# Kernel tuning notes

Hardware: AMD Instinct MI355X
Metric: run time of the kernel (lower is better)

## Reference

```python
import jax, jax.numpy as jnp
from jax import lax
import numpy as np

B, C_IN, HW = 4096, 3, 32
D = 256          # feature/output dim
E = 16           # num experts
H = 1024         # expert hidden dim
K = 2            # top-k
NC = 1000        # num classes


def _conv(x, w, b):
    # x: NCHW, w: OIHW, stride 1, SAME padding
    y = lax.conv_general_dilated(x, w, (1, 1), 'SAME',
                                 dimension_numbers=('NCHW', 'OIHW', 'NCHW'))
    return y + b[None, :, None, None]


def _maxpool2(x):
    return lax.reduce_window(x, -jnp.inf, lax.max, (1, 1, 2, 2), (1, 1, 2, 2), 'VALID')


def setup_inputs() -> dict:
    key = jax.random.key(0)
    ks = jax.random.split(key, 16)
    s = lambda *sh: 1.0 / np.sqrt(sh[-2] if len(sh) > 1 else sh[0])
    inp = {
        'x':       jax.random.normal(ks[0], (B, C_IN, HW, HW), jnp.float32),
        'conv1_w': jax.random.normal(ks[1], (32, 3, 3, 3), jnp.float32) * 0.1,
        'conv1_b': jnp.zeros((32,), jnp.float32),
        'conv2_w': jax.random.normal(ks[2], (64, 32, 3, 3), jnp.float32) * 0.05,
        'conv2_b': jnp.zeros((64,), jnp.float32),
        'conv3_w': jax.random.normal(ks[3], (128, 64, 3, 3), jnp.float32) * 0.04,
        'conv3_b': jnp.zeros((128,), jnp.float32),
        'fc_w':    jax.random.normal(ks[4], (128 * 4 * 4, D), jnp.float32) * (1.0 / np.sqrt(2048)),
        'fc_b':    jnp.zeros((D,), jnp.float32),
        'gate_w':  jax.random.normal(ks[5], (D, E), jnp.float32) * (1.0 / np.sqrt(D)),
        'gate_b':  jnp.zeros((E,), jnp.float32),
        'e_w1':    jax.random.normal(ks[6], (E, D, H), jnp.float32) * (1.0 / np.sqrt(D)),
        'e_b1':    jnp.zeros((E, H), jnp.float32),
        'e_w2':    jax.random.normal(ks[7], (E, H, D), jnp.float32) * (1.0 / np.sqrt(H)),
        'e_b2':    jnp.zeros((E, D), jnp.float32),
        'ln_g':    jnp.ones((D,), jnp.float32),
        'ln_b':    jnp.zeros((D,), jnp.float32),
        'out_w':   jax.random.normal(ks[8], (D, NC), jnp.float32) * (1.0 / np.sqrt(D)),
        'out_b':   jnp.zeros((NC,), jnp.float32),
    }
    return inp


def reference(x, conv1_w, conv1_b, conv2_w, conv2_b, conv3_w, conv3_b,
              fc_w, fc_b, gate_w, gate_b, e_w1, e_b1, e_w2, e_b2,
              ln_g, ln_b, out_w, out_b):
    # --- CNN feature extractor: conv -> maxpool -> relu, x3 ---
    h = jax.nn.relu(_maxpool2(_conv(x, conv1_w, conv1_b)))   # [B,32,16,16]
    h = jax.nn.relu(_maxpool2(_conv(h, conv2_w, conv2_b)))   # [B,64,8,8]
    h = jax.nn.relu(_maxpool2(_conv(h, conv3_w, conv3_b)))   # [B,128,4,4]
    feat = h.reshape(h.shape[0], -1) @ fc_w + fc_b           # [B,D]

    # --- Gating: top-k softmax scattered into sparse [B,E] ---
    logits = feat @ gate_w + gate_b                          # [B,E]
    topk_vals, topk_idx = lax.top_k(logits, K)               # [B,K]
    gate_w_k = jax.nn.softmax(topk_vals, axis=-1)            # [B,K]
    gates = jnp.zeros_like(logits).at[jnp.arange(feat.shape[0])[:, None], topk_idx].set(gate_w_k)

    # --- Dense all-expert compute, masked combine (faithful to source) ---
    h1 = jax.nn.relu(jnp.einsum('bd,edh->beh', feat, e_w1) + e_b1[None])   # [B,E,H]
    eo = jnp.einsum('beh,ehd->bed', h1, e_w2) + e_b2[None]                 # [B,E,D]
    moe = jnp.einsum('be,bed->bd', gates, eo)                              # [B,D]

    D_i = gates.mean(axis=0)
    lb_loss = jnp.sum(D_i * jnp.log(D_i + 1e-8))

    # --- LayerNorm(residual) ---
    y = moe + feat
    mu = y.mean(-1, keepdims=True)
    var = y.var(-1, keepdims=True)
    y = (y - mu) / jnp.sqrt(var + 1e-5) * ln_g + ln_b

    out = y @ out_w + out_b                                   # [B,NC]
    return out, lb_loss
```

## Files before the change

kernel.cpp:

```cpp
#include <hip/hip_runtime.h>
#include <hip/hip_bf16.h>

typedef short bf16x8 __attribute__((ext_vector_type(8)));
typedef float f32x4 __attribute__((ext_vector_type(4)));

#define NB   4096
#define NEXP 16
#define DDIM 256
#define HDIM 1024
#define NCLS 1000

#define OFF_B    ((size_t)0)
#define OFF_P0   ((size_t)0)
#define OFF_P1   ((size_t)4194304)
#define OFF_W1TH ((size_t)8388608)
#define OFF_W1TL ((size_t)16777216)
#define OFF_W2TH ((size_t)25165824)
#define OFF_W2TL ((size_t)33554432)
#define OFF_WFCH ((size_t)41943040)
#define OFF_WFCL ((size_t)42991616)
#define OFF_P2   ((size_t)44040192)
#define OFF_P3   ((size_t)48234496)
#define OFF_OWH  ((size_t)52428800)
#define OFF_OWL  ((size_t)53477376)
#define OFF_CHH  ((size_t)67108864)
#define OFF_CHL  ((size_t)83886080)
#define OFF_WBL  ((size_t)67145728)
#define OFF_WA1H ((size_t)67182592)
#define OFF_WA1L ((size_t)67184640)
#define OFF_FEAT ((size_t)100663296)
#define OFF_WAL  ((size_t)100810752)
#define OFF_MOE  ((size_t)104857600)
#define OFF_CNT  ((size_t)109051904)
#define OFF_GSUM ((size_t)109051968)
#define OFF_LROW ((size_t)109052032)
#define OFF_LG   ((size_t)109314176)

__device__ inline unsigned short f2bf(float v) {
  __hip_bfloat16 h = __float2bfloat16(v);
  return *(unsigned short*)&h;
}
__device__ inline float bf2f(unsigned short u) {
  union { unsigned int i; float f; } c; c.i = ((unsigned int)u) << 16; return c.f;
}

__global__ __launch_bounds__(256) void k_wt1b(const float* __restrict__ w,
    unsigned short* __restrict__ oh, unsigned short* __restrict__ ol) {
  int i = blockIdx.x*256 + threadIdx.x;
  if (i >= 1024) return;
  int k = i & 31, oc = i >> 5;
  float v = (k < 27) ? w[oc*27 + k] : 0.f;
  unsigned short h = f2bf(v);
  oh[i] = h;
  ol[i] = f2bf(v - bf2f(h));
}

__global__ __launch_bounds__(256) void k_wt2b(const float* __restrict__ w,
    unsigned short* __restrict__ wBh, unsigned short* __restrict__ wBl) {
  int i = blockIdx.x*256 + threadIdx.x;
  if (i >= 9*64*32) return;
  int ic = i & 31, rem = i >> 5;
  int oc = rem & 63, tap = rem >> 6;
  float v = w[(oc*32 + ic)*9 + tap];
  unsigned short h = f2bf(v);
  wBh[i] = h;
  wBl[i] = f2bf(v - bf2f(h));
}

__global__ __launch_bounds__(256) void k_pack(const float* __restrict__ in,
    unsigned short* __restrict__ oh, unsigned short* __restrict__ ol, int R, int C) {
  __shared__ float tile[64][65];
  const int t = threadIdx.x;
  const int e = blockIdx.z;
  const size_t eb = (size_t)e * R * C;
  const int c0 = blockIdx.x*64, r0 = blockIdx.y*64;
  const int cc = t & 63, r4 = t >> 6;
  #pragma unroll
  for (int j = 0; j < 16; ++j) {
    int rr = r4 + j*4;
    tile[rr][cc] = in[eb + (size_t)(r0+rr)*C + c0 + cc];
  }
  __syncthreads();
  const int K32 = R >> 5;
  #pragma unroll
  for (int j = 0; j < 16; ++j) {
    int idx = t + j*256;
    int jin = idx & 7, lane = (idx >> 3) & 63, ksl = (idx >> 9) & 1, ntl = idx >> 10;
    int kl = ksl*32 + ((lane >> 4) << 3) + jin;
    int nl = ntl*16 + (lane & 15);
    float v = tile[kl][nl];
    unsigned short h = f2bf(v);
    size_t o = eb + ((size_t)(((c0 >> 4) + ntl)*K32 + (r0 >> 5) + ksl)*64 + lane)*8 + jin;
    oh[o] = h;
    ol[o] = f2bf(v - bf2f(h));
  }
}

__global__ __launch_bounds__(256) void k_packo(const float* __restrict__ ow,
    unsigned short* __restrict__ oh, unsigned short* __restrict__ ol) {
  int i = blockIdx.x*256 + threadIdx.x;
  int j = i & 7, lane = (i >> 3) & 63, ks = (i >> 9) & 7, nt = i >> 12;
  int k = ks*32 + ((lane >> 4) << 3) + j;
  int n = nt*16 + (lane & 15);
  float v = (n < NCLS) ? ow[(size_t)k*NCLS + n] : 0.f;
  unsigned short h = f2bf(v);
  oh[i] = h;
  ol[i] = f2bf(v - bf2f(h));
}

__global__ __launch_bounds__(512, 4) void k_conv12(const float* __restrict__ x,
    const unsigned short* __restrict__ wA1h, const unsigned short* __restrict__ wA1l,
    const float* __restrict__ b1,
    const unsigned short* __restrict__ wBh, const unsigned short* __restrict__ wBl,
    const float* __restrict__ b2, float* __restrict__ outB) {
  __shared__ unsigned int xsu[3*34*36];
  __shared__ unsigned short ishB[2][10368];
  __shared__ float bs1[32];
  __shared__ float bs2[64];
  const int t = threadIdx.x;
  const int img = blockIdx.x;
  for (int i = t; i < 3*34*36; i += 512) xsu[i] = 0u;
  {
    unsigned int* z = (unsigned int*)&ishB[0][0];
    for (int i = t; i < 10368; i += 512) z[i] = 0u;
  }
  __syncthreads();
  for (int i = t; i < 3072; i += 512) {
    int ic = i >> 10, rem = i & 1023, y = rem >> 5, xx = rem & 31;
    float v = x[(size_t)img*3072 + i];
    unsigned short h = f2bf(v);
    unsigned short l = f2bf(v - bf2f(h));
    xsu[ic*34*36 + (y+1)*36 + (xx+1)] = ((unsigned int)l << 16) | (unsigned int)h;
  }
  if (t < 32) bs1[t] = b1[t];
  else if (t >= 64 && t < 128) bs2[t-64] = b2[t-64];

  const int lane = t & 63, wvv = t >> 6;
  const int lr = lane & 15, lq = lane >> 4;

  const int oct1 = wvv & 1;
  const bf16x8 a1h = *(const bf16x8*)&wA1h[((oct1*16 + lr) << 5) + lq*8];
  const bf16x8 a1l = *(const bf16x8*)&wA1l[((oct1*16 + lr) << 5) + lq*8];

  int koff[8];
  #pragma unroll
  for (int j = 0; j < 8; ++j) {
    int k = lq*8 + j;
    if (k < 27) {
      int ic = k/9, tap = k - ic*9, dy = tap/3, dx = tap - dy*3;
      koff[j] = ic*34*36 + dy*36 + dx;
    } else koff[j] = -1;
  }
  __syncthreads();

  {
    const int rp  = wvv >> 1;
    const int ly0 = (rp >> 1) << 1;
    const int xh  = rp & 1;
    const int X   = xh*16 + lr;
    for (int ps = 0; ps < 8; ++ps) {
      const int baseA = (ps*4 + ly0)*36 + X;
      union { unsigned int u[4]; bf16x8 v; } bhA, blA, bhB, blB;
      #pragma unroll
      for (int jj = 0; jj < 4; ++jj) {
        unsigned int e0A = (koff[2*jj]   >= 0) ? xsu[koff[2*jj]   + baseA] : 0u;
        unsigned int e1A = (koff[2*jj+1] >= 0) ? xsu[koff[2*jj+1] + baseA] : 0u;
        unsigned int e0B = (koff[2*jj]   >= 0) ? xsu[koff[2*jj]   + baseA + 36] : 0u;
        unsigned int e1B = (koff[2*jj+1] >= 0) ? xsu[koff[2*jj+1] + baseA + 36] : 0u;
        bhA.u[jj] = __builtin_amdgcn_perm(e1A, e0A, 0x05040100u);
        blA.u[jj] = __builtin_amdgcn_perm(e1A, e0A, 0x07060302u);
        bhB.u[jj] = __builtin_amdgcn_perm(e1B, e0B, 0x05040100u);
        blB.u[jj] = __builtin_amdgcn_perm(e1B, e0B, 0x07060302u);
      }
      f32x4 aA = (f32x4){0.f,0.f,0.f,0.f}, aB = (f32x4){0.f,0.f,0.f,0.f};
      aA = __builtin_amdgcn_mfma_f32_16x16x32_bf16(a1h, bhA.v, aA, 0, 0, 0);
      aB = __builtin_amdgcn_mfma_f32_16x16x32_bf16(a1h, bhB.v, aB, 0, 0, 0);
      aA = __builtin_amdgcn_mfma_f32_16x16x32_bf16(a1h, blA.v, aA, 0, 0, 0);
      aB = __builtin_amdgcn_mfma_f32_16x16x32_bf16(a1h, blB.v, aB, 0, 0, 0);
      aA = __builtin_amdgcn_mfma_f32_16x16x32_bf16(a1l, bhA.v, aA, 0, 0, 0);
      aB = __builtin_amdgcn_mfma_f32_16x16x32_bf16(a1l, bhB.v, aB, 0, 0, 0);
      #pragma unroll
      for (int r = 0; r < 4; ++r) {
        float v = fmaxf(aA[r], aB[r]);
        v = fmaxf(v, __shfl_xor(v, 1, 64));
        if ((lr & 1) == 0) {
          int oc = oct1*16 + lq*4 + r;
          int Xp = xh*8 + (lr >> 1);
          int Yp = ps*2 + (ly0 >> 1);
          float m = fmaxf(v + bs1[oc], 0.f);
          unsigned short h = f2bf(m);
          unsigned short l = f2bf(m - bf2f(h));
          int pl = (Yp+1)*18 + (Xp+1);
          int sl = pl*4 + ((oc >> 3) ^ ((pl >> 1) & 3));
          int us = (sl << 3) | (oc & 7);
          ishB[0][us] = h; ishB[1][us] = l;
        }
      }
    }
  }
  __syncthreads();
  {
    const int mtp = (wvv & 1)*2;
    const int rq = wvv >> 1;
    f32x4 acc[2][4];
    #pragma unroll
    for (int i = 0; i < 2; ++i)
      #pragma unroll
      for (int j = 0; j < 4; ++j) acc[i][j] = (f32x4){0.f,0.f,0.f,0.f};
    bf16x8 nAh[2], nAl[2];
    #pragma unroll
    for (int m = 0; m < 2; ++m) {
      int off = (((mtp+m)*16 + lr) << 5) + lq*8;
      nAh[m] = *(const bf16x8*)&wBh[off];
      nAl[m] = *(const bf16x8*)&wBl[off];
    }
    #pragma unroll
    for (int tap = 0; tap < 9; ++tap) {
      bf16x8 ah0 = nAh[0], al0 = nAl[0], ah1 = nAh[1], al1 = nAl[1];
      if (tap < 8) {
        #pragma unroll
        for (int m = 0; m < 2; ++m) {
          int off = (((tap+1)*64 + (mtp+m)*16 + lr) << 5) + lq*8;
          nAh[m] = *(const bf16x8*)&wBh[off];
          nAl[m] = *(const bf16x8*)&wBl[off];
        }
      }
      const int dy = tap/3, dx = tap - dy*3;
      #pragma unroll
      for (int j = 0; j < 4; ++j) {
        int pl = (rq*4 + j + dy)*18 + lr + dx;
        int sl = pl*4 + (lq ^ ((pl >> 1) & 3));
        bf16x8 bh = *(const bf16x8*)&ishB[0][sl << 3];
        bf16x8 bl = *(const bf16x8*)&ishB[1][sl << 3];
        acc[0][j] = __builtin_amdgcn_mfma_f32_16x16x32_bf16(ah0, bh, acc[0][j], 0, 0, 0);
        acc[1][j] = __builtin_amdgcn_mfma_f32_16x16x32_bf16(ah1, bh, acc[1][j], 0, 0, 0);
        acc[0][j] = __builtin_amdgcn_mfma_f32_16x16x32_bf16(ah0, bl, acc[0][j], 0, 0, 0);
        acc[1][j] = __builtin_amdgcn_mfma_f32_16x16x32_bf16(ah1, bl, acc[1][j], 0, 0, 0);
        acc[0][j] = __builtin_amdgcn_mfma_f32_16x16x32_bf16(al0, bh, acc[0][j], 0, 0, 0);
        acc[1][j] = __builtin_amdgcn_mfma_f32_16x16x32_bf16(al1, bh, acc[1][j], 0, 0, 0);
      }
    }
    __syncthreads();
    float* ps2 = (float*)&ishB[0][0];
    #pragma unroll
    for (int m = 0; m < 2; ++m)
      #pragma unroll
      for (int k = 0; k < 2; ++k)
        #pragma unroll
        for (int r = 0; r < 4; ++r) {
          float v = fmaxf(acc[m][2*k][r], acc[m][2*k+1][r]);
          v = fmaxf(v, __shfl_xor(v, 1, 64));
          if ((lr & 1) == 0) {
            int oc = (mtp + m)*16 + lq*4 + r;
            int Y = rq*2 + k, X = lr >> 1;
            ps2[oc*65 + Y*8 + X] = fmaxf(v + bs2[oc], 0.f);
          }
        }
    __syncthreads();
    float* op = outB + (size_t)img*4096;
    #pragma unroll
    for (int jj = 0; jj < 8; ++jj) {
      int i = jj*512 + t;
      op[i] = ps2[(i >> 6)*65 + (i & 63)];
    }
  }
}

__global__ __launch_bounds__(256) void k_wt3b(const float* __restrict__ w,
    unsigned short* __restrict__ wAh, unsigned short* __restrict__ wAl) {
  int i = blockIdx.x*256 + threadIdx.x;
  if (i >= 9*128*64) return;
  int ic = i & 63, rem = i >> 6;
  int oc = rem & 127, tap = rem >> 7;
  float v = w[(oc*64 + ic)*9 + tap];
  unsigned short h = f2bf(v);
  wAh[i] = h;
  wAl[i] = f2bf(v - bf2f(h));
}

__global__ __launch_bounds__(256) void k_conv3(const float* __restrict__ inB,
    const unsigned short* __restrict__ wAh, const unsigned short* __restrict__ wAl,
    const float* __restrict__ bias,
    unsigned short* __restrict__ Chh, unsigned short* __restrict__ Chl) {
  __shared__ unsigned short ish[2][6400];
  const int t = threadIdx.x;
  const int img = blockIdx.x;
  {
    unsigned int* z = (unsigned int*)&ish[0][0];
    #pragma unroll
    for (int j = 0; j < 25; ++j) z[t + 256*j] = 0u;
  }
  __syncthreads();
  {
    const float* src = inB + (size_t)img*4096;
    #pragma unroll
    for (int j = 0; j < 16; ++j) {
      int f = t + 256*j;
      int ic = f >> 6, p = f & 63;
      int pl = ((p >> 3) + 1)*10 + (p & 7) + 1;
      float v = src[f];
      unsigned short h = f2bf(v);
      unsigned short l = f2bf(v - bf2f(h));
      int u = pl*64 + ic;
      int us = (((u >> 3) ^ (pl & 7)) << 3) | (u & 7);
      ish[0][us] = h; ish[1][us] = l;
    }
  }
  __syncthreads();

  const int lane = t & 63, wid = t >> 6;
  const int lr = lane & 15, lq = lane >> 4;
  const int mt0 = wid*2;
  const int yb = lr >> 3, xb = lr & 7;

  f32x4 acc[2][4];
  #pragma unroll
  for (int i = 0; i < 2; ++i)
    #pragma unroll
    for (int j = 0; j < 4; ++j) acc[i][j] = (f32x4){0.f,0.f,0.f,0.f};

  for (int tap = 0; tap < 9; ++tap) {
    const int dy = tap/3, dx = tap - dy*3;
    #pragma unroll
    for (int kc = 0; kc < 2; ++kc) {
      const int kb = kc*32 + lq*8;
      const int wbase = ((tap << 7) << 6) + kb;
      bf16x8 a0h = *(const bf16x8*)&wAh[wbase + ((mt0*16 + lr) << 6)];
      bf16x8 a0l = *(const bf16x8*)&wAl[wbase + ((mt0*16 + lr) << 6)];
      bf16x8 a1h = *(const bf16x8*)&wAh[wbase + (((mt0+1)*16 + lr) << 6)];
      bf16x8 a1l = *(const bf16x8*)&wAl[wbase + (((mt0+1)*16 + lr) << 6)];
      #pragma unroll
      for (int nt = 0; nt < 4; ++nt) {
        const int pl = (2*nt + yb + dy)*10 + xb + dx;
        const int u = pl*64 + kb;
        const int us = (((u >> 3) ^ (pl & 7)) << 3);
        bf16x8 bh = *(const bf16x8*)&ish[0][us];
        bf16x8 bl = *(const bf16x8*)&ish[1][us];
        acc[0][nt] = __builtin_amdgcn_mfma_f32_16x16x32_bf16(a0h, bh, acc[0][nt], 0, 0, 0);
        acc[0][nt] = __builtin_amdgcn_mfma_f32_16x16x32_bf16(a0h, bl, acc[0][nt], 0, 0, 0);
        acc[0][nt] = __builtin_amdgcn_mfma_f32_16x16x32_bf16(a0l, bh, acc[0][nt], 0, 0, 0);
        acc[1][nt] = __builtin_amdgcn_mfma_f32_16x16x32_bf16(a1h, bh, acc[1][nt], 0, 0, 0);
        acc[1][nt] = __builtin_amdgcn_mfma_f32_16x16x32_bf16(a1h, bl, acc[1][nt], 0, 0, 0);
        acc[1][nt] = __builtin_amdgcn_mfma_f32_16x16x32_bf16(a1l, bh, acc[1][nt], 0, 0, 0);
      }
    }
  }
  __syncthreads();
  float* stg = (float*)&ish[0][0];
  #pragma unroll
  for (int mtl = 0; mtl < 2; ++mtl)
    #pragma unroll
    for (int nt = 0; nt < 4; ++nt)
      #pragma unroll
      for (int r = 0; r < 4; ++r) {
        float v = acc[mtl][nt][r];
        v = fmaxf(v, __shfl_xor(v, 1, 64));
        v = fmaxf(v, __shfl_xor(v, 8, 64));
        if ((lane & 9) == 0) {
          int oc = (mt0 + mtl)*16 + lq*4 + r;
          int pix = nt*4 + (xb >> 1);
          stg[oc*17 + pix] = fmaxf(v + bias[oc], 0.f);
        }
      }
  __syncthreads();
  #pragma unroll
  for (int j = 0; j < 8; ++j) {
    int i = t + 256*j;
    float v = stg[(i >> 4)*17 + (i & 15)];
    unsigned short h = f2bf(v);
    Chh[(size_t)img*2048 + i] = h;
    Chl[(size_t)img*2048 + i] = f2bf(v - bf2f(h));
  }
}

__global__ __launch_bounds__(256) void k_fc(const unsigned short* __restrict__ Chh,
    const unsigned short* __restrict__ Chl,
    const unsigned short* __restrict__ wfh, const unsigned short* __restrict__ wfl,
    float* __restrict__ P0, float* __restrict__ P1,
    float* __restrict__ P2, float* __restrict__ P3) {
  const int t = threadIdx.x;
  const int r0 = blockIdx.x * 32;
  const int kq = blockIdx.z;
  float* __restrict__ P = (kq == 0) ? P0 : (kq == 1) ? P1 : (kq == 2) ? P2 : P3;
  const int lane = t & 63, wv = t >> 6;
  const int lr = lane & 15, lq = lane >> 4;
  f32x4 acc[2][4];
  #pragma unroll
  for (int i = 0; i < 2; ++i)
    #pragma unroll
    for (int j = 0; j < 4; ++j) acc[i][j] = (f32x4){0.f,0.f,0.f,0.f};
  #pragma unroll 4
  for (int ks = 0; ks < 16; ++ks) {
    bf16x8 ah[2], al[2];
    #pragma unroll
    for (int rt = 0; rt < 2; ++rt) {
      size_t ao = (size_t)(r0 + rt*16 + lr)*2048 + kq*512 + ks*32 + lq*8;
      ah[rt] = *(const bf16x8*)&Chh[ao];
      al[rt] = *(const bf16x8*)&Chl[ao];
    }
    #pragma unroll
    for (int nt = 0; nt < 4; ++nt) {
      size_t bo = ((size_t)((wv*4 + nt)*64 + kq*16 + ks)*64 + lane)*8;
      bf16x8 bh = *(const bf16x8*)&wfh[bo];
      bf16x8 bl = *(const bf16x8*)&wfl[bo];
      acc[0][nt] = __builtin_amdgcn_mfma_f32_16x16x32_bf16(ah[0], bh, acc[0][nt], 0, 0, 0);
      acc[1][nt] = __builtin_amdgcn_mfma_f32_16x16x32_bf16(ah[1], bh, acc[1][nt], 0, 0, 0);
      acc[0][nt] = __builtin_amdgcn_mfma_f32_16x16x32_bf16(ah[0], bl, acc[0][nt], 0, 0, 0);
      acc[1][nt] = __builtin_amdgcn_mfma_f32_16x16x32_bf16(ah[1], bl, acc[1][nt], 0, 0, 0);
      acc[0][nt] = __builtin_amdgcn_mfma_f32_16x16x32_bf16(al[0], bh, acc[0][nt], 0, 0, 0);
      acc[1][nt] = __builtin_amdgcn_mfma_f32_16x16x32_bf16(al[1], bh, acc[1][nt], 0, 0, 0);
    }
  }
  #pragma unroll
  for (int rt = 0; rt < 2; ++rt)
    #pragma unroll
    for (int nt = 0; nt < 4; ++nt)
      #pragma unroll
      for (int r = 0; r < 4; ++r)
        P[(size_t)(r0 + rt*16 + lq*4 + r)*256 + (wv*4 + nt)*16 + lr] = acc[rt][nt][r];
}

__global__ __launch_bounds__(256) void k_gate(const float* __restrict__ P0,
    const float* __restrict__ P1, const float* __restrict__ P2, const float* __restrict__ P3,
    const float* __restrict__ fcb,
    const float* __restrict__ gw, const float* __restrict__ gb,
    float* __restrict__ feat, int* __restrict__ cnt, float* __restrict__ gsum,
    int* __restrict__ lrow, float* __restrict__ lg) {
  __shared__ float ft[16][256];
  __shared__ float lgs[16][16];
  __shared__ float gwl[4096];
  const int t = threadIdx.x;
  const int r0 = blockIdx.x * 16;
  for (int i = t; i < 4096; i += 256) gwl[i] = gw[i];
  float bb = fcb[t];
  #pragma unroll
  for (int r = 0; r < 16; ++r) {
    size_t off = (size_t)(r0+r)*256 + t;
    float v = P0[off] + P1[off] + P2[off] + P3[off] + bb;
    ft[r][t] = v;
    feat[off] = v;
  }
  __syncthreads();
  {
    int r = t >> 4, e = t & 15;
    float s = gb[e];
    for (int k = 0; k < 256; ++k) s = fmaf(ft[r][k], gwl[k*16 + e], s);
    lgs[r][e] = s;
  }
  __syncthreads();
  if (t < 16) {
    int r = t;
    float v1 = -3.402823e38f, v2 = -3.402823e38f;
    int i1 = 0, i2 = 0;
    for (int e = 0; e < 16; ++e) {
      float v = lgs[r][e];
      if (v > v1)      { v2 = v1; i2 = i1; v1 = v; i1 = e; }
      else if (v > v2) { v2 = v;  i2 = e; }
    }
    float ex = __expf(v2 - v1);
    float g1 = 1.f / (1.f + ex);
    float g2 = ex  / (1.f + ex);
    int row = r0 + r;
    int p1 = atomicAdd(&cnt[i1], 1); lrow[i1*4096 + p1] = row; lg[i1*4096 + p1] = g1;
    int p2 = atomicAdd(&cnt[i2], 1); lrow[i2*4096 + p2] = row; lg[i2*4096 + p2] = g2;
    atomicAdd(&gsum[i1], g1);
    atomicAdd(&gsum[i2], g2);
  }
}

__global__ __launch_bounds__(256) void k_moe(const float* __restrict__ feat,
    const unsigned short* __restrict__ w1th, const unsigned short* __restrict__ w1tl,
    const unsigned short* __restrict__ w2th, const unsigned short* __restrict__ w2tl,
    const float* __restrict__ eb1, const float* __restrict__ eb2,
    const int* __restrict__ cnt, const int* __restrict__ lrow, const float* __restrict__ lgw,
    float* __restrict__ moe) {
  const int e = blockIdx.y;
  const int n_e = cnt[e];
  const int start = blockIdx.x * 32;
  if (start >= n_e) return;
  const int c = blockIdx.z;
  const int n = min(32, n_e - start);
  __shared__ unsigned short fh[8192], fl[8192];
  __shared__ unsigned short h1h[4096], h1l[4096];
  __shared__ int   rws[32];
  __shared__ float gws[32];
  const int t = threadIdx.x;
  if (t < 32) {
    rws[t] = (t < n) ? lrow[e*4096 + start + t] : 0;
    gws[t] = (t < n) ? lgw[e*4096 + start + t] : 0.f;
  }
  __syncthreads();
  for (int j = 0; j < 32; ++j) {
    float v = (j < n) ? feat[(size_t)rws[j]*256 + t] : 0.f;
    unsigned short h = f2bf(v);
    int us = (j*32 + ((t >> 3) ^ (j & 7)))*8 + (t & 7);
    fh[us] = h; fl[us] = f2bf(v - bf2f(h));
  }
  const int lane = t & 63, wv = t >> 6;
  const int lr = lane & 15, lq = lane >> 4;
  const int rh = wv & 1, qh = wv >> 1;
  const int arow = rh*16 + lr;
  const int rsw = arow & 7;
  const size_t ewb = (size_t)e << 18;

  f32x4 acc2[8];
  #pragma unroll
  for (int i = 0; i < 8; ++i) acc2[i] = (f32x4){0.f,0.f,0.f,0.f};

  __syncthreads();

  {
    f32x4 acc1[4];
    #pragma unroll
    for (int i = 0; i < 4; ++i) acc1[i] = (f32x4){0.f,0.f,0.f,0.f};
    #pragma unroll
    for (int ks = 0; ks < 8; ++ks) {
      int aoff = (arow*32 + ((ks*4 + lq) ^ rsw))*8;
      bf16x8 ah = *(const bf16x8*)&fh[aoff];
      bf16x8 al = *(const bf16x8*)&fl[aoff];
      #pragma unroll
      for (int ht = 0; ht < 4; ++ht) {
        int htile = c*8 + qh*4 + ht;
        size_t bo = ewb + ((size_t)(htile*8 + ks)*64 + lane)*8;
        bf16x8 bh = *(const bf16x8*)&w1th[bo];
        bf16x8 bl = *(const bf16x8*)&w1tl[bo];
        acc1[ht] = __builtin_amdgcn_mfma_f32_16x16x32_bf16(ah, bh, acc1[ht], 0, 0, 0);
        acc1[ht] = __builtin_amdgcn_mfma_f32_16x16x32_bf16(ah, bl, acc1[ht], 0, 0, 0);
        acc1[ht] = __builtin_amdgcn_mfma_f32_16x16x32_bf16(al, bh, acc1[ht], 0, 0, 0);
      }
    }
    __syncthreads();
    #pragma unroll
    for (int ht = 0; ht < 4; ++ht) {
      int hloc = qh*64 + ht*16 + lr;
      float bb = eb1[e*1024 + c*128 + hloc];
      #pragma unroll
      for (int r = 0; r < 4; ++r) {
        int orow = rh*16 + lq*4 + r;
        float v = fmaxf(acc1[ht][r] + bb, 0.f);
        unsigned short hh = f2bf(v);
        int us = (orow*16 + ((hloc >> 3) ^ (orow & 7)))*8 + (hloc & 7);
        h1h[us] = hh; h1l[us] = f2bf(v - bf2f(hh));
      }
    }
    __syncthreads();
    #pragma unroll
    for (int ks = 0; ks < 4; ++ks) {
      int aoff = (arow*16 + ((ks*4 + lq) ^ rsw))*8;
      bf16x8 ah = *(const bf16x8*)&h1h[aoff];
      bf16x8 al = *(const bf16x8*)&h1l[aoff];
      #pragma unroll
      for (int dt = 0; dt < 8; ++dt) {
        int dtile = qh*8 + dt;
        size_t bo = ewb + ((size_t)(dtile*32 + c*4 + ks)*64 + lane)*8;
        bf16x8 bh = *(const bf16x8*)&w2th[bo];
        bf16x8 bl = *(const bf16x8*)&w2tl[bo];
        acc2[dt] = __builtin_amdgcn_mfma_f32_16x16x32_bf16(ah, bh, acc2[dt], 0, 0, 0);
        acc2[dt] = __builtin_amdgcn_mfma_f32_16x16x32_bf16(ah, bl, acc2[dt], 0, 0, 0);
        acc2[dt] = __builtin_amdgcn_mfma_f32_16x16x32_bf16(al, bh, acc2[dt], 0, 0, 0);
      }
    }
  }
  #pragma unroll
  for (int dt = 0; dt < 8; ++dt) {
    int d = qh*128 + dt*16 + lr;
    float b2 = (c == 0) ? eb2[e*256 + d] : 0.f;
    #pragma unroll
    for (int r = 0; r < 4; ++r) {
      int orow = rh*16 + lq*4 + r;
      if (orow < n)
        atomicAdd(&moe[(size_t)rws[orow]*256 + d], gws[orow]*(acc2[dt][r] + b2));
    }
  }
}

__global__ void k_lb(const float* __restrict__ gsum, float* __restrict__ out_lb) {
  int t = threadIdx.x;
  float term = 0.f;
  if (t < 16) {
    float D = gsum[t] * (1.f/4096.f);
    term = D * logf(D + 1e-8f);
  }
  #pragma unroll
  for (int o = 8; o > 0; o >>= 1) term += __shfl_down(term, o, 64);
  if (t == 0) *out_lb = term;
}

__global__ __launch_bounds__(256) void k_ln(const float* __restrict__ feat,
    const float* __restrict__ moe, const float* __restrict__ g, const float* __restrict__ bp,
    unsigned short* __restrict__ yh, unsigned short* __restrict__ yl) {
  const int r = blockIdx.x, t = threadIdx.x;
  float v = moe[(size_t)r*256 + t] + feat[(size_t)r*256 + t];
  float s = v, q = v * v;
  #pragma unroll
  for (int o = 32; o > 0; o >>= 1) {
    s += __shfl_down(s, o, 64);
    q += __shfl_down(q, o, 64);
  }
  __shared__ float ss[4], qq[4];
  int wv = t >> 6;
  if ((t & 63) == 0) { ss[wv] = s; qq[wv] = q; }
  __syncthreads();
  float S = ss[0]+ss[1]+ss[2]+ss[3];
  float Q = qq[0]+qq[1]+qq[2]+qq[3];
  float mu  = S * (1.f/256.f);
  float var = Q * (1.f/256.f) - mu*mu;
  float inv = rsqrtf(var + 1e-5f);
  float y = (v - mu) * inv * g[t] + bp[t];
  unsigned short h = f2bf(y);
  yh[(size_t)r*256 + t] = h;
  yl[(size_t)r*256 + t] = f2bf(y - bf2f(h));
}

__global__ __launch_bounds__(256) void k_out(const unsigned short* __restrict__ yh,
    const unsigned short* __restrict__ yl,
    const unsigned short* __restrict__ owh, const unsigned short* __restrict__ owl,
    const float* __restrict__ ob, float* __restrict__ out) {
  const int t = threadIdx.x;
  const int r0 = blockIdx.x * 32;
  const int lane = t & 63, wv = t >> 6;
  const int lr = lane & 15, lq = lane >> 4;
  const int ntile = blockIdx.y*4 + wv;
  f32x4 acc[2];
  acc[0] = (f32x4){0.f,0.f,0.f,0.f};
  acc[1] = (f32x4){0.f,0.f,0.f,0.f};
  #pragma unroll
  for (int ks = 0; ks < 8; ++ks) {
    bf16x8 bh = *(const bf16x8*)&owh[((size_t)(ntile*8 + ks)*64 + lane)*8];
    bf16x8 bl = *(const bf16x8*)&owl[((size_t)(ntile*8 + ks)*64 + lane)*8];
    #pragma unroll
    for (int rt = 0; rt < 2; ++rt) {
      size_t ao = (size_t)(r0 + rt*16 + lr)*256 + ks*32 + lq*8;
      bf16x8 ah = *(const bf16x8*)&yh[ao];
      bf16x8 al = *(const bf16x8*)&yl[ao];
      acc[rt] = __builtin_amdgcn_mfma_f32_16x16x32_bf16(ah, bh, acc[rt], 0, 0, 0);
      acc[rt] = __builtin_amdgcn_mfma_f32_16x16x32_bf16(ah, bl, acc[rt], 0, 0, 0);
      acc[rt] = __builtin_amdgcn_mfma_f32_16x16x32_bf16(al, bh, acc[rt], 0, 0, 0);
    }
  }
  const int col = ntile*16 + lr;
  if (col < NCLS) {
    float bb = ob[col];
    #pragma unroll
    for (int rt = 0; rt < 2; ++rt)
      #pragma unroll
      for (int r = 0; r < 4; ++r)
        out[(size_t)(r0 + rt*16 + lq*4 + r)*NCLS + col] = acc[rt][r] + bb;
  }
}

extern "C" void kernel_launch(void* const* d_in, const int* in_sizes, int n_in,
                              void* d_out, int out_size, void* d_ws, size_t ws_size,
                              hipStream_t stream) {
  const float* x   = (const float*)d_in[0];
  const float* c1w = (const float*)d_in[1];
  const float* c1b = (const float*)d_in[2];
  const float* c2w = (const float*)d_in[3];
  const float* c2b = (const float*)d_in[4];
  const float* c3w = (const float*)d_in[5];
  const float* c3b = (const float*)d_in[6];
  const float* fcw = (const float*)d_in[7];
  const float* fcb = (const float*)d_in[8];
  const float* gw  = (const float*)d_in[9];
  const float* gb  = (const float*)d_in[10];
  const float* ew1 = (const float*)d_in[11];
  const float* eb1 = (const float*)d_in[12];
  const float* ew2 = (const float*)d_in[13];
  const float* eb2 = (const float*)d_in[14];
  const float* lng = (const float*)d_in[15];
  const float* lnb = (const float*)d_in[16];
  const float* ow  = (const float*)d_in[17];
  const float* ob  = (const float*)d_in[18];
  char* ws = (char*)d_ws;
  float* Bb   = (float*)(ws + OFF_B);
  float* P0   = (float*)(ws + OFF_P0);
  float* P1   = (float*)(ws + OFF_P1);
  float* P2   = (float*)(ws + OFF_P2);
  float* P3   = (float*)(ws + OFF_P3);
  unsigned short* Chh = (unsigned short*)(ws + OFF_CHH);
  unsigned short* Chl = (unsigned short*)(ws + OFF_CHL);
  unsigned short* wBh = (unsigned short*)(ws + OFF_CHH);
  unsigned short* wBl = (unsigned short*)(ws + OFF_WBL);
  unsigned short* wA1h = (unsigned short*)(ws + OFF_WA1H);
  unsigned short* wA1l = (unsigned short*)(ws + OFF_WA1L);
  unsigned short* wAh = (unsigned short*)(ws + OFF_FEAT);
  unsigned short* wAl = (unsigned short*)(ws + OFF_WAL);
  unsigned short* w1th = (unsigned short*)(ws + OFF_W1TH);
  unsigned short* w1tl = (unsigned short*)(ws + OFF_W1TL);
  unsigned short* w2th = (unsigned short*)(ws + OFF_W2TH);
  unsigned short* w2tl = (unsigned short*)(ws + OFF_W2TL);
  unsigned short* wfh = (unsigned short*)(ws + OFF_WFCH);
  unsigned short* wfl = (unsigned short*)(ws + OFF_WFCL);
  unsigned short* owph = (unsigned short*)(ws + OFF_OWH);
  unsigned short* owpl = (unsigned short*)(ws + OFF_OWL);
  unsigned short* yh = (unsigned short*)(ws + OFF_P0);
  unsigned short* yl = (unsigned short*)(ws + OFF_P1);
  float* feat = (float*)(ws + OFF_FEAT);
  float* moe  = (float*)(ws + OFF_MOE);
  int*   cnt  = (int*)(ws + OFF_CNT);
  float* gsum = (float*)(ws + OFF_GSUM);
  int*   lrow = (int*)(ws + OFF_LROW);
  float* lgv  = (float*)(ws + OFF_LG);
  float* outp = (float*)d_out;

  hipMemsetAsync(ws + OFF_MOE, 0, 4194304 + 128, stream);

  hipLaunchKernelGGL(k_wt1b,   dim3(4),       dim3(256), 0, stream, c1w, wA1h, wA1l);
  hipLaunchKernelGGL(k_wt2b,   dim3(72),      dim3(256), 0, stream, c2w, wBh, wBl);
  hipLaunchKernelGGL(k_wt3b,   dim3(288),     dim3(256), 0, stream, c3w, wAh, wAl);
  hipLaunchKernelGGL(k_conv12, dim3(4096),    dim3(512), 0, stream, x, wA1h, wA1l, c1b, wBh, wBl, c2b, Bb);
  hipLaunchKernelGGL(k_conv3,  dim3(4096),    dim3(256), 0, stream, Bb, wAh, wAl, c3b, Chh, Chl);
  hipLaunchKernelGGL(k_pack,   dim3(16, 4, 16), dim3(256), 0, stream, ew1, w1th, w1tl, 256, 1024);
  hipLaunchKernelGGL(k_pack,   dim3(4, 16, 16), dim3(256), 0, stream, ew2, w2th, w2tl, 1024, 256);
  hipLaunchKernelGGL(k_pack,   dim3(4, 32, 1),  dim3(256), 0, stream, fcw, wfh, wfl, 2048, 256);
  hipLaunchKernelGGL(k_packo,  dim3(1024),    dim3(256), 0, stream, ow, owph, owpl);
  hipLaunchKernelGGL(k_fc,     dim3(128, 1, 4), dim3(256), 0, stream, Chh, Chl, wfh, wfl, P0, P1, P2, P3);
  hipLaunchKernelGGL(k_gate,   dim3(256),     dim3(256), 0, stream, P0, P1, P2, P3, fcb, gw, gb,
                     feat, cnt, gsum, lrow, lgv);
  hipLaunchKernelGGL(k_moe,    dim3(128, 16, 8), dim3(256), 0, stream, feat, w1th, w1tl, w2th, w2tl,
                     eb1, eb2, cnt, lrow, lgv, moe);
  hipLaunchKernelGGL(k_lb,     dim3(1),       dim3(64),  0, stream, gsum, outp + (size_t)NB*NCLS);
  hipLaunchKernelGGL(k_ln,     dim3(4096),    dim3(256), 0, stream, feat, moe, lng, lnb, yh, yl);
  hipLaunchKernelGGL(k_out,    dim3(128, 16), dim3(256), 0, stream, yh, yl, owph, owpl, ob, outp);
}
```

Baseline: 808.7 us.

## Fuse conv3 into conv1-2 kernel, keeping pooled activations in LDS

```diff
diff --git a/kernel.cpp b/kernel.cpp
--- a/kernel.cpp
+++ b/kernel.cpp
@@ -10,7 +10,6 @@
 #define HDIM 1024
 #define NCLS 1000
 
-#define OFF_B    ((size_t)0)
 #define OFF_P0   ((size_t)0)
 #define OFF_P1   ((size_t)4194304)
 #define OFF_W1TH ((size_t)8388608)
@@ -25,11 +24,13 @@
 #define OFF_OWL  ((size_t)53477376)
 #define OFF_CHH  ((size_t)67108864)
 #define OFF_CHL  ((size_t)83886080)
-#define OFF_WBL  ((size_t)67145728)
-#define OFF_WA1H ((size_t)67182592)
-#define OFF_WA1L ((size_t)67184640)
 #define OFF_FEAT ((size_t)100663296)
+#define OFF_WAH  ((size_t)100663296)
 #define OFF_WAL  ((size_t)100810752)
+#define OFF_WB2H ((size_t)100958208)
+#define OFF_WB2L ((size_t)100995072)
+#define OFF_WA1H ((size_t)101031936)
+#define OFF_WA1L ((size_t)101033984)
 #define OFF_MOE  ((size_t)104857600)
 #define OFF_CNT  ((size_t)109051904)
 #define OFF_GSUM ((size_t)109051968)
@@ -67,6 +68,18 @@
   wBl[i] = f2bf(v - bf2f(h));
 }
 
+__global__ __launch_bounds__(256) void k_wt3b(const float* __restrict__ w,
+    unsigned short* __restrict__ wAh, unsigned short* __restrict__ wAl) {
+  int i = blockIdx.x*256 + threadIdx.x;
+  if (i >= 9*128*64) return;
+  int ic = i & 63, rem = i >> 6;
+  int oc = rem & 127, tap = rem >> 7;
+  float v = w[(oc*64 + ic)*9 + tap];
+  unsigned short h = f2bf(v);
+  wAh[i] = h;
+  wAl[i] = f2bf(v - bf2f(h));
+}
+
 __global__ __launch_bounds__(256) void k_pack(const float* __restrict__ in,
     unsigned short* __restrict__ oh, unsigned short* __restrict__ ol, int R, int C) {
   __shared__ float tile[64][65];
@@ -108,18 +121,22 @@
   ol[i] = f2bf(v - bf2f(h));
 }
 
-__global__ __launch_bounds__(512, 4) void k_conv12(const float* __restrict__ x,
+__global__ __launch_bounds__(512, 4) void k_conv123(const float* __restrict__ x,
     const unsigned short* __restrict__ wA1h, const unsigned short* __restrict__ wA1l,
     const float* __restrict__ b1,
     const unsigned short* __restrict__ wBh, const unsigned short* __restrict__ wBl,
-    const float* __restrict__ b2, float* __restrict__ outB) {
-  __shared__ unsigned int xsu[3*34*36];
+    const float* __restrict__ b2,
+    const unsigned short* __restrict__ wAh, const unsigned short* __restrict__ wAl,
+    const float* __restrict__ b3,
+    unsigned short* __restrict__ Chh, unsigned short* __restrict__ Chl) {
+  __shared__ unsigned int xsu[4*34*36];
   __shared__ unsigned short ishB[2][10368];
   __shared__ float bs1[32];
   __shared__ float bs2[64];
+  __shared__ float bs3[128];
   const int t = threadIdx.x;
   const int img = blockIdx.x;
-  for (int i = t; i < 3*34*36; i += 512) xsu[i] = 0u;
+  for (int i = t; i < 4*34*36; i += 512) xsu[i] = 0u;
   {
     unsigned int* z = (unsigned int*)&ishB[0][0];
     for (int i = t; i < 10368; i += 512) z[i] = 0u;
@@ -130,10 +147,11 @@
     float v = x[(size_t)img*3072 + i];
     unsigned short h = f2bf(v);
     unsigned short l = f2bf(v - bf2f(h));
-    xsu[ic*34*36 + (y+1)*36 + (xx+1)] = ((unsigned int)l << 16) | (unsigned int)h;
+    xsu[ic*1224 + (y+1)*36 + (xx+1)] = ((unsigned int)l << 16) | (unsigned int)h;
   }
   if (t < 32) bs1[t] = b1[t];
   else if (t >= 64 && t < 128) bs2[t-64] = b2[t-64];
+  else if (t >= 128 && t < 256) bs3[t-128] = b3[t-128];
 
   const int lane = t & 63, wvv = t >> 6;
   const int lr = lane & 15, lq = lane >> 4;
@@ -146,10 +164,8 @@
   #pragma unroll
   for (int j = 0; j < 8; ++j) {
     int k = lq*8 + j;
-    if (k < 27) {
-      int ic = k/9, tap = k - ic*9, dy = tap/3, dx = tap - dy*3;
-      koff[j] = ic*34*36 + dy*36 + dx;
-    } else koff[j] = -1;
+    int ic = k/9, tap = k - ic*9, dy = tap/3, dx = tap - dy*3;
+    koff[j] = ic*1224 + dy*36 + dx;
   }
   __syncthreads();
 
@@ -163,10 +179,10 @@
       union { unsigned int u[4]; bf16x8 v; } bhA, blA, bhB, blB;
       #pragma unroll
       for (int jj = 0; jj < 4; ++jj) {
-        unsigned int e0A = (koff[2*jj]   >= 0) ? xsu[koff[2*jj]   + baseA] : 0u;
-        unsigned int e1A = (koff[2*jj+1] >= 0) ? xsu[koff[2*jj+1] + baseA] : 0u;
-        unsigned int e0B = (koff[2*jj]   >= 0) ? xsu[koff[2*jj]   + baseA + 36] : 0u;
-        unsigned int e1B = (koff[2*jj+1] >= 0) ? xsu[koff[2*jj+1] + baseA + 36] : 0u;
+        unsigned int e0A = xsu[koff[2*jj]   + baseA];
+        unsigned int e1A = xsu[koff[2*jj+1] + baseA];
+        unsigned int e0B = xsu[koff[2*jj]   + baseA + 36];
+        unsigned int e1B = xsu[koff[2*jj+1] + baseA + 36];
         bhA.u[jj] = __builtin_amdgcn_perm(e1A, e0A, 0x05040100u);
         blA.u[jj] = __builtin_amdgcn_perm(e1A, e0A, 0x07060302u);
         bhB.u[jj] = __builtin_amdgcn_perm(e1B, e0B, 0x05040100u);
@@ -199,10 +215,10 @@
     }
   }
   __syncthreads();
+  f32x4 acc[2][4];
   {
     const int mtp = (wvv & 1)*2;
     const int rq = wvv >> 1;
-    f32x4 acc[2][4];
     #pragma unroll
     for (int i = 0; i < 2; ++i)
       #pragma unroll
@@ -240,8 +256,19 @@
         acc[1][j] = __builtin_amdgcn_mfma_f32_16x16x32_bf16(al1, bh, acc[1][j], 0, 0, 0);
       }
     }
-    __syncthreads();
-    float* ps2 = (float*)&ishB[0][0];
+  }
+  __syncthreads();
+  {
+    unsigned int* z0 = (unsigned int*)&ishB[0][0];
+    unsigned int* z1 = (unsigned int*)&ishB[1][0];
+    for (int i = t; i < 3200; i += 512) { z0[i] = 0u; z1[i] = 0u; }
+  }
+  __syncthreads();
+  {
+    const int mtp = (wvv & 1)*2;
+    const int rq = wvv >> 1;
+    unsigned short* ish0 = &ishB[0][0];
+    unsigned short* ish1 = &ishB[1][0];
     #pragma unroll
     for (int m = 0; m < 2; ++m)
       #pragma unroll
@@ -251,125 +278,73 @@
           float v = fmaxf(acc[m][2*k][r], acc[m][2*k+1][r]);
           v = fmaxf(v, __shfl_xor(v, 1, 64));
           if ((lr & 1) == 0) {
-            int oc = (mtp + m)*16 + lq*4 + r;
+            int ic = (mtp + m)*16 + lq*4 + r;
             int Y = rq*2 + k, X = lr >> 1;
-            ps2[oc*65 + Y*8 + X] = fmaxf(v + bs2[oc], 0.f);
+            float vv = fmaxf(v + bs2[ic], 0.f);
+            unsigned short h = f2bf(vv);
+            unsigned short l = f2bf(vv - bf2f(h));
+            int pl = (Y+1)*10 + (X+1);
+            int u = pl*64 + ic;
+            int us = (((u >> 3) ^ (pl & 7)) << 3) | (u & 7);
+            ish0[us] = h; ish1[us] = l;
           }
         }
-    __syncthreads();
-    float* op = outB + (size_t)img*4096;
-    #pragma unroll
-    for (int jj = 0; jj < 8; ++jj) {
-      int i = jj*512 + t;
-      op[i] = ps2[(i >> 6)*65 + (i & 63)];
-    }
-  }
-}
-
-__global__ __launch_bounds__(256) void k_wt3b(const float* __restrict__ w,
-    unsigned short* __restrict__ wAh, unsigned short* __restrict__ wAl) {
-  int i = blockIdx.x*256 + threadIdx.x;
-  if (i >= 9*128*64) return;
-  int ic = i & 63, rem = i >> 6;
-  int oc = rem & 127, tap = rem >> 7;
-  float v = w[(oc*64 + ic)*9 + tap];
-  unsigned short h = f2bf(v);
-  wAh[i] = h;
-  wAl[i] = f2bf(v - bf2f(h));
-}
-
-__global__ __launch_bounds__(256) void k_conv3(const float* __restrict__ inB,
-    const unsigned short* __restrict__ wAh, const unsigned short* __restrict__ wAl,
-    const float* __restrict__ bias,
-    unsigned short* __restrict__ Chh, unsigned short* __restrict__ Chl) {
-  __shared__ unsigned short ish[2][6400];
-  const int t = threadIdx.x;
-  const int img = blockIdx.x;
-  {
-    unsigned int* z = (unsigned int*)&ish[0][0];
-    #pragma unroll
-    for (int j = 0; j < 25; ++j) z[t + 256*j] = 0u;
-  }
-  __syncthreads();
-  {
-    const float* src = inB + (size_t)img*4096;
-    #pragma unroll
-    for (int j = 0; j < 16; ++j) {
-      int f = t + 256*j;
-      int ic = f >> 6, p = f & 63;
-      int pl = ((p >> 3) + 1)*10 + (p & 7) + 1;
-      float v = src[f];
-      unsigned short h = f2bf(v);
-      unsigned short l = f2bf(v - bf2f(h));
-      int u = pl*64 + ic;
-      int us = (((u >> 3) ^ (pl & 7)) << 3) | (u & 7);
-      ish[0][us] = h; ish[1][us] = l;
-    }
-  }
-  __syncthreads();
-
-  const int lane = t & 63, wid = t >> 6;
-  const int lr = lane & 15, lq = lane >> 4;
-  const int mt0 = wid*2;
-  const int yb = lr >> 3, xb = lr & 7;
-
-  f32x4 acc[2][4];
-  #pragma unroll
-  for (int i = 0; i < 2; ++i)
-    #pragma unroll
-    for (int j = 0; j < 4; ++j) acc[i][j] = (f32x4){0.f,0.f,0.f,0.f};
-
-  for (int tap = 0; tap < 9; ++tap) {
-    const int dy = tap/3, dx = tap - dy*3;
-    #pragma unroll
-    for (int kc = 0; kc < 2; ++kc) {
-      const int kb = kc*32 + lq*8;
-      const int wbase = ((tap << 7) << 6) + kb;
-      bf16x8 a0h = *(const bf16x8*)&wAh[wbase + ((mt0*16 + lr) << 6)];
-      bf16x8 a0l = *(const bf16x8*)&wAl[wbase + ((mt0*16 + lr) << 6)];
-      bf16x8 a1h = *(const bf16x8*)&wAh[wbase + (((mt0+1)*16 + lr) << 6)];
-      bf16x8 a1l = *(const bf16x8*)&wAl[wbase + (((mt0+1)*16 + lr) << 6)];
-      #pragma unroll
-      for (int nt = 0; nt < 4; ++nt) {
-        const int pl = (2*nt + yb + dy)*10 + xb + dx;
-        const int u = pl*64 + kb;
-        const int us = (((u >> 3) ^ (pl & 7)) << 3);
-        bf16x8 bh = *(const bf16x8*)&ish[0][us];
-        bf16x8 bl = *(const bf16x8*)&ish[1][us];
-        acc[0][nt] = __builtin_amdgcn_mfma_f32_16x16x32_bf16(a0h, bh, acc[0][nt], 0, 0, 0);
-        acc[0][nt] = __builtin_amdgcn_mfma_f32_16x16x32_bf16(a0h, bl, acc[0][nt], 0, 0, 0);
-        acc[0][nt] = __builtin_amdgcn_mfma_f32_16x16x32_bf16(a0l, bh, acc[0][nt], 0, 0, 0);
-        acc[1][nt] = __builtin_amdgcn_mfma_f32_16x16x32_bf16(a1h, bh, acc[1][nt], 0, 0, 0);
-        acc[1][nt] = __builtin_amdgcn_mfma_f32_16x16x32_bf16(a1h, bl, acc[1][nt], 0, 0, 0);
-        acc[1][nt] = __builtin_amdgcn_mfma_f32_16x16x32_bf16(a1l, bh, acc[1][nt], 0, 0, 0);
-      }
-    }
-  }
-  __syncthreads();
-  float* stg = (float*)&ish[0][0];
-  #pragma unroll
-  for (int mtl = 0; mtl < 2; ++mtl)
+  }
+  __syncthreads();
+  {
+    const unsigned short* ish0 = &ishB[0][0];
+    const unsigned short* ish1 = &ishB[1][0];
+    const int yb = lr >> 3, xb = lr & 7;
+    f32x4 acc3[4];
+    #pragma unroll
+    for (int i = 0; i < 4; ++i) acc3[i] = (f32x4){0.f,0.f,0.f,0.f};
+    for (int tap = 0; tap < 9; ++tap) {
+      const int dy = tap/3, dx = tap - dy*3;
+      #pragma unroll
+      for (int kc = 0; kc < 2; ++kc) {
+        const int kb = kc*32 + lq*8;
+        const int wbase = ((tap << 7) << 6) + kb;
+        bf16x8 a_h = *(const bf16x8*)&wAh[wbase + ((wvv*16 + lr) << 6)];
+        bf16x8 a_l = *(const bf16x8*)&wAl[wbase + ((wvv*16 + lr) << 6)];
+        #pragma unroll
+        for (int nt = 0; nt < 4; ++nt) {
+          const int pl = (2*nt + yb + dy)*10 + xb + dx;
+          const int u = pl*64 + kb;
+          const int us = (((u >> 3) ^ (pl & 7)) << 3);
+          bf16x8 bh = *(const bf16x8*)&ish0[us];
+          bf16x8 bl = *(const bf16x8*)&ish1[us];
+          acc3[nt] = __builtin_amdgcn_mfma_f32_16x16x32_bf16(a_h, bh, acc3[nt], 0, 0, 0);
+          acc3[nt] = __builtin_amdgcn_mfma_f32_16x16x32_bf16(a_h, bl, acc3[nt], 0, 0, 0);
+          acc3[nt] = __builtin_amdgcn_mfma_f32_16x16x32_bf16(a_l, bh, acc3[nt], 0, 0, 0);
+        }
+      }
+    }
+    float* stg = (float*)&xsu[0];
     #pragma unroll
     for (int nt = 0; nt < 4; ++nt)
       #pragma unroll
       for (int r = 0; r < 4; ++r) {
-        float v = acc[mtl][nt][r];
+        float v = acc3[nt][r];
         v = fmaxf(v, __shfl_xor(v, 1, 64));
         v = fmaxf(v, __shfl_xor(v, 8, 64));
         if ((lane & 9) == 0) {
-          int oc = (mt0 + mtl)*16 + lq*4 + r;
+          int oc = wvv*16 + lq*4 + r;
           int pix = nt*4 + (xb >> 1);
-          stg[oc*17 + pix] = fmaxf(v + bias[oc], 0.f);
+          stg[oc*17 + pix] = fmaxf(v + bs3[oc], 0.f);
         }
       }
-  __syncthreads();
-  #pragma unroll
-  for (int j = 0; j < 8; ++j) {
-    int i = t + 256*j;
-    float v = stg[(i >> 4)*17 + (i & 15)];
-    unsigned short h = f2bf(v);
-    Chh[(size_t)img*2048 + i] = h;
-    Chl[(size_t)img*2048 + i] = f2bf(v - bf2f(h));
+  }
+  __syncthreads();
+  {
+    const float* stg = (const float*)&xsu[0];
+    #pragma unroll
+    for (int j = 0; j < 4; ++j) {
+      int i = t + 512*j;
+      float v = stg[(i >> 4)*17 + (i & 15)];
+      unsigned short h = f2bf(v);
+      Chh[(size_t)img*2048 + i] = h;
+      Chl[(size_t)img*2048 + i] = f2bf(v - bf2f(h));
+    }
   }
 }
 
@@ -672,19 +647,18 @@
   const float* ow  = (const float*)d_in[17];
   const float* ob  = (const float*)d_in[18];
   char* ws = (char*)d_ws;
-  float* Bb   = (float*)(ws + OFF_B);
   float* P0   = (float*)(ws + OFF_P0);
   float* P1   = (float*)(ws + OFF_P1);
   float* P2   = (float*)(ws + OFF_P2);
   float* P3   = (float*)(ws + OFF_P3);
   unsigned short* Chh = (unsigned short*)(ws + OFF_CHH);
   unsigned short* Chl = (unsigned short*)(ws + OFF_CHL);
-  unsigned short* wBh = (unsigned short*)(ws + OFF_CHH);
-  unsigned short* wBl = (unsigned short*)(ws + OFF_WBL);
+  unsigned short* wAh = (unsigned short*)(ws + OFF_WAH);
+  unsigned short* wAl = (unsigned short*)(ws + OFF_WAL);
+  unsigned short* wBh = (unsigned short*)(ws + OFF_WB2H);
+  unsigned short* wBl = (unsigned short*)(ws + OFF_WB2L);
   unsigned short* wA1h = (unsigned short*)(ws + OFF_WA1H);
   unsigned short* wA1l = (unsigned short*)(ws + OFF_WA1L);
-  unsigned short* wAh = (unsigned short*)(ws + OFF_FEAT);
-  unsigned short* wAl = (unsigned short*)(ws + OFF_WAL);
   unsigned short* w1th = (unsigned short*)(ws + OFF_W1TH);
   unsigned short* w1tl = (unsigned short*)(ws + OFF_W1TL);
   unsigned short* w2th = (unsigned short*)(ws + OFF_W2TH);
@@ -708,12 +682,12 @@
   hipLaunchKernelGGL(k_wt1b,   dim3(4),       dim3(256), 0, stream, c1w, wA1h, wA1l);
   hipLaunchKernelGGL(k_wt2b,   dim3(72),      dim3(256), 0, stream, c2w, wBh, wBl);
   hipLaunchKernelGGL(k_wt3b,   dim3(288),     dim3(256), 0, stream, c3w, wAh, wAl);
-  hipLaunchKernelGGL(k_conv12, dim3(4096),    dim3(512), 0, stream, x, wA1h, wA1l, c1b, wBh, wBl, c2b, Bb);
-  hipLaunchKernelGGL(k_conv3,  dim3(4096),    dim3(256), 0, stream, Bb, wAh, wAl, c3b, Chh, Chl);
   hipLaunchKernelGGL(k_pack,   dim3(16, 4, 16), dim3(256), 0, stream, ew1, w1th, w1tl, 256, 1024);
   hipLaunchKernelGGL(k_pack,   dim3(4, 16, 16), dim3(256), 0, stream, ew2, w2th, w2tl, 1024, 256);
   hipLaunchKernelGGL(k_pack,   dim3(4, 32, 1),  dim3(256), 0, stream, fcw, wfh, wfl, 2048, 256);
   hipLaunchKernelGGL(k_packo,  dim3(1024),    dim3(256), 0, stream, ow, owph, owpl);
+  hipLaunchKernelGGL(k_conv123, dim3(4096),   dim3(512), 0, stream, x, wA1h, wA1l, c1b,
+                     wBh, wBl, c2b, wAh, wAl, c3b, Chh, Chl);
   hipLaunchKernelGGL(k_fc,     dim3(128, 1, 4), dim3(256), 0, stream, Chh, Chl, wfh, wfl, P0, P1, P2, P3);
   hipLaunchKernelGGL(k_gate,   dim3(256),     dim3(256), 0, stream, P0, P1, P2, P3, fcb, gw, gb,
                      feat, cnt, gsum, lrow, lgv);
```

Measured after the change: 979.5 us. +21.1%, slower.
